# Kernel optimization log

Measured on AMD Instinct MI355X. Metric: run time of the kernel, lower is better.

## Reference

```python
import jax, jax.numpy as jnp
import numpy as np

B, T, C, H = 2, 2048, 1024, 16
HD = C // H  # head dim = 64


def setup_inputs() -> dict:
    key = jax.random.key(0)
    ks = jax.random.split(key, 5)
    s = 0.02  # GPT-style init scale for weights
    return {
        "x": jax.random.normal(ks[0], (B, T, C), dtype=jnp.float32),
        "Wq": jax.random.normal(ks[1], (C, C), dtype=jnp.float32) * s,
        "bq": jnp.zeros((C,), dtype=jnp.float32),
        "Wk": jax.random.normal(ks[2], (C, C), dtype=jnp.float32) * s,
        "bk": jnp.zeros((C,), dtype=jnp.float32),
        "Wv": jax.random.normal(ks[3], (C, C), dtype=jnp.float32) * s,
        "bv": jnp.zeros((C,), dtype=jnp.float32),
        "Wp": jax.random.normal(ks[4], (C, C), dtype=jnp.float32) * s,
        "bp": jnp.zeros((C,), dtype=jnp.float32),
    }


def reference(x, Wq, bq, Wk, bk, Wv, bv, Wp, bp):
    b, t, c = x.shape
    # torch nn.Linear: y = x @ W.T + b  (W is [out, in])
    def heads(W, bias):
        y = jnp.einsum("btc,oc->bto", x, W) + bias
        return y.reshape(b, t, H, HD).transpose(0, 2, 1, 3)  # [B,H,T,hd]

    q = heads(Wq, bq)
    k = heads(Wk, bk)
    v = heads(Wv, bv)

    scale = 1.0 / np.sqrt(HD).astype(np.float32)
    att = jnp.einsum("bhqd,bhkd->bhqk", q, k) * scale  # [B,H,T,T]
    causal = jnp.tril(jnp.ones((t, t), dtype=bool))
    att = jnp.where(causal[None, None], att, -jnp.inf)
    att = jax.nn.softmax(att, axis=-1)
    # attn_pdrop = 0.0 -> dropout is identity
    y = jnp.einsum("bhqk,bhkd->bhqd", att, v)  # [B,H,T,hd]
    y = y.transpose(0, 2, 1, 3).reshape(b, t, c)
    y = jnp.einsum("btc,oc->bto", y, Wp) + bp  # resid_pdrop = 0.0
    return y
```

## Files before the change

### kernel.cpp

```cpp
#include <hip/hip_runtime.h>
#include <hip/hip_bf16.h>

using bf16 = __hip_bfloat16;
typedef __attribute__((ext_vector_type(8))) short short8;
typedef __attribute__((ext_vector_type(4))) float floatx4;

#define B_  2
#define T_  2048
#define C_  1024
#define H_  16
#define HD_ 64
#define BT_ (B_*T_)
#define NX_ ((size_t)BT_*C_)
#define NW_ ((size_t)C_*C_)
#define PSTR2 40
#define KSCQ 0.1803368801f

__device__ __forceinline__ void gl2lds16(const bf16* g, bf16* l) {
    __builtin_amdgcn_global_load_lds((const __attribute__((address_space(1))) unsigned int*)g,
                                     (__attribute__((address_space(3))) unsigned int*)l,
                                     16, 0, 0);
}

__global__ __launch_bounds__(256) void cvt_f32_bf16(
    const float* __restrict__ x,
    const float* __restrict__ Wq, const float* __restrict__ Wk,
    const float* __restrict__ Wv, const float* __restrict__ Wp,
    bf16* __restrict__ xb, bf16* __restrict__ wqb, bf16* __restrict__ wkb,
    bf16* __restrict__ wvb, bf16* __restrict__ wpb)
{
    size_t i4 = ((size_t)blockIdx.x * 256 + threadIdx.x) * 4;
    const float* src; bf16* dst; size_t off;
    if (i4 < NX_) { src = x; dst = xb; off = i4; }
    else {
        size_t j = i4 - NX_;
        int r = (int)(j >> 20);
        off = j & (NW_ - 1);
        src = (r==0) ? Wq : (r==1) ? Wk : (r==2) ? Wv : Wp;
        dst = (r==0) ? wqb : (r==1) ? wkb : (r==2) ? wvb : wpb;
    }
    float4 v = *(const float4*)(src + off);
    union { bf16 h[4]; uint2 u; } o;
    o.h[0] = __float2bfloat16(v.x); o.h[1] = __float2bfloat16(v.y);
    o.h[2] = __float2bfloat16(v.z); o.h[3] = __float2bfloat16(v.w);
    *(uint2*)(dst + off) = o.u;
}

__global__ __launch_bounds__(256) void qkv_gemm(
    const bf16* __restrict__ x,
    const bf16* __restrict__ Wq, const float* __restrict__ bq,
    const bf16* __restrict__ Wk, const float* __restrict__ bk,
    const bf16* __restrict__ Wv, const float* __restrict__ bv,
    bf16* __restrict__ qo, bf16* __restrict__ ko, bf16* __restrict__ vt)
{
    __shared__ __align__(16) bf16 As[128*32];
    __shared__ __align__(16) bf16 Bs[128*32];

    const int tid  = threadIdx.x;
    const int w    = tid >> 6, lane = tid & 63;
    const int g    = lane >> 4, c16 = lane & 15;
    const int wr   = w >> 1,    wc  = w & 1;
    const int mtile = blockIdx.x, ntile = blockIdx.y;
    const int wsel  = ntile >> 3;
    const bf16*  W    = (wsel==0) ? Wq : (wsel==1 ? Wk : Wv);
    const float* bias = (wsel==0) ? bq : (wsel==1 ? bk : bv);
    const float oscale = (wsel==0) ? KSCQ : 1.0f;
    const int nbase  = (ntile & 7) * 128;

    const bf16* ag = x + (size_t)(mtile*128)*C_;
    const bf16* bg = W + (size_t)nbase*C_;

    floatx4 acc[4][4] = {};

    for (int k0 = 0; k0 < C_; k0 += 32) {
        #pragma unroll
        for (int p = 0; p < 2; ++p) {
            int cb = p*256 + w*64;
            int c  = cb + lane;
            gl2lds16(ag + (size_t)(c>>2)*C_ + k0 + (c&3)*8, As + cb*8);
            gl2lds16(bg + (size_t)(c>>2)*C_ + k0 + (c&3)*8, Bs + cb*8);
        }
        __syncthreads();

        short8 af[4], bfr[4];
        #pragma unroll
        for (int i = 0; i < 4; ++i)
            af[i] = *(const short8*)(As + (wr*64 + i*16 + c16)*32 + g*8);
        #pragma unroll
        for (int j = 0; j < 4; ++j)
            bfr[j] = *(const short8*)(Bs + (wc*64 + j*16 + c16)*32 + g*8);
        #pragma unroll
        for (int i = 0; i < 4; ++i)
            #pragma unroll
            for (int j = 0; j < 4; ++j)
                acc[i][j] = __builtin_amdgcn_mfma_f32_16x16x32_bf16(af[i], bfr[j], acc[i][j], 0, 0, 0);
        __syncthreads();
    }

    #pragma unroll
    for (int i = 0; i < 4; ++i) {
        int m0 = mtile*128 + wr*64 + i*16 + g*4;
        #pragma unroll
        for (int j = 0; j < 4; ++j) {
            int n = nbase + wc*64 + j*16 + c16;
            float bvf = bias[n];
            if (wsel == 2) {
                int bb = m0 >> 11, t0 = m0 & (T_-1);
                int hh = n >> 6,  hd = n & 63;
                union { bf16 hv[4]; uint2 u; } tmp;
                #pragma unroll
                for (int r = 0; r < 4; ++r) tmp.hv[r] = __float2bfloat16(acc[i][j][r] + bvf);
                *(uint2*)(vt + ((size_t)((bb*H_ + hh)*64 + hd))*T_ + t0) = tmp.u;
            } else {
                bf16* dst = (wsel==0) ? qo : ko;
                #pragma unroll
                for (int r = 0; r < 4; ++r)
                    dst[(size_t)(m0+r)*C_ + n] = __float2bfloat16((acc[i][j][r] + bvf) * oscale);
            }
        }
    }
}

__global__ __launch_bounds__(256, 4) void attn(
    const bf16* __restrict__ q, const bf16* __restrict__ k,
    const bf16* __restrict__ vt, bf16* __restrict__ y)
{
    __shared__ __align__(16) bf16 Ks[16*512];
    __shared__ __align__(16) bf16 Vs[16*512];
    __shared__ __align__(16) bf16 Ps[4][16*PSTR2];

    const int tid = threadIdx.x, w = tid >> 6, lane = tid & 63;
    const int g = lane >> 4, c16 = lane & 15;
    const int beta = blockIdx.x;
    const int p = beta & 15;
    const int h = (beta >> 4) & 15;
    const int b = beta >> 8;

    const bf16* kbase = k  + ((size_t)(b*T_))*C_ + h*64;
    const bf16* vbase = vt + ((size_t)(b*H_ + h))*64*T_;

    const short ONEB = 0x3F80;
    const short8 ones = {ONEB,ONEB,ONEB,ONEB,ONEB,ONEB,ONEB,ONEB};

    for (int ph = 0; ph < 2; ++ph) {
        const int qt = ph ? 31 - p : p;
        const int qbase = qt*64 + w*16;
        const int nit = (qt + 2) >> 1;
        const int qglob = qbase + c16;

        short8 aq[2];
        #pragma unroll
        for (int kg = 0; kg < 2; ++kg)
            aq[kg] = *(const short8*)(q + ((size_t)(b*T_ + qglob))*C_ + h*64 + kg*32 + g*8);

        floatx4 accO[4] = {};
        floatx4 lacc = {};

        for (int kt = 0; kt < nit; ++kt) {
            #pragma unroll
            for (int p2 = 0; p2 < 4; ++p2) {
                int f = w*4 + p2;
                int ctk = f >> 1, kg = f & 1;
                gl2lds16(kbase + (size_t)(kt*128 + ctk*16 + c16)*C_ + kg*32 + g*8, Ks + f*512);
                gl2lds16(vbase + (size_t)(p2*16 + c16)*T_ + kt*128 + w*32 + g*8,   Vs + f*512);
            }
            __syncthreads();

            floatx4 s[8];
            #pragma unroll
            for (int ct = 0; ct < 8; ++ct) {
                floatx4 a = {0.f, 0.f, 0.f, 0.f};
                #pragma unroll
                for (int kg = 0; kg < 2; ++kg) {
                    short8 kb = *(const short8*)(Ks + (ct*2 + kg)*512 + lane*8);
                    a = __builtin_amdgcn_mfma_f32_16x16x32_bf16(kb, aq[kg], a, 0, 0, 0);
                }
                s[ct] = a;
            }

            if (kt == nit-1) {
                #pragma unroll
                for (int ct = 0; ct < 8; ++ct)
                    #pragma unroll
                    for (int r = 0; r < 4; ++r) {
                        int key = kt*128 + ct*16 + g*4 + r;
                        if (key > qglob) s[ct][r] = -1e30f;
                    }
            }

            #pragma unroll
            for (int ks = 0; ks < 4; ++ks) {
                #pragma unroll
                for (int half = 0; half < 2; ++half) {
                    int ct = ks*2 + half;
                    float p0 = exp2f(s[ct][0]);
                    float p1 = exp2f(s[ct][1]);
                    float p2 = exp2f(s[ct][2]);
                    float p3 = exp2f(s[ct][3]);
                    union { __hip_bfloat162 h2[2]; uint2 u; } pk;
                    pk.h2[0] = __float22bfloat162_rn(float2{p0, p1});
                    pk.h2[1] = __float22bfloat162_rn(float2{p2, p3});
                    *(uint2*)(Ps[w] + c16*PSTR2 + half*16 + g*4) = pk.u;
                }
                short8 pa = *(const short8*)(Ps[w] + c16*PSTR2 + g*8);
                lacc = __builtin_amdgcn_mfma_f32_16x16x32_bf16(pa, ones, lacc, 0, 0, 0);
                #pragma unroll
                for (int nt = 0; nt < 4; ++nt) {
                    short8 vb = *(const short8*)(Vs + (ks*4 + nt)*512 + lane*8);
                    accO[nt] = __builtin_amdgcn_mfma_f32_16x16x32_bf16(pa, vb, accO[nt], 0, 0, 0);
                }
            }
            __syncthreads();
        }

        float ir[4];
        #pragma unroll
        for (int r = 0; r < 4; ++r) ir[r] = __builtin_amdgcn_rcpf(lacc[r]);
        #pragma unroll
        for (int nt = 0; nt < 4; ++nt)
            #pragma unroll
            for (int r = 0; r < 4; ++r) {
                int row = qbase + g*4 + r;
                float o = accO[nt][r] * ir[r];
                y[((size_t)(b*T_ + row))*C_ + h*64 + nt*16 + c16] = __float2bfloat16(o);
            }
    }
}

__global__ __launch_bounds__(256) void proj_gemm(
    const bf16* __restrict__ yin, const bf16* __restrict__ Wp, const float* __restrict__ bp,
    float* __restrict__ out)
{
    __shared__ __align__(16) bf16 As[64*32];
    __shared__ __align__(16) bf16 Bs[128*32];

    const int tid = threadIdx.x;
    const int w = tid >> 6, lane = tid & 63;
    const int g = lane >> 4, c16 = lane & 15;
    const int mtile = blockIdx.x, ntile = blockIdx.y;
    const int nbase = ntile * 128;

    const bf16* ag = yin + (size_t)(mtile*64)*C_;
    const bf16* bg = Wp  + (size_t)nbase*C_;

    floatx4 acc[4][2] = {};

    for (int k0 = 0; k0 < C_; k0 += 32) {
        gl2lds16(ag + (size_t)(w*16 + (lane>>2))*C_ + k0 + (lane&3)*8, As + w*512);
        #pragma unroll
        for (int p = 0; p < 2; ++p) {
            int cb = p*256 + w*64;
            int c  = cb + lane;
            gl2lds16(bg + (size_t)(c>>2)*C_ + k0 + (c&3)*8, Bs + cb*8);
        }
        __syncthreads();

        short8 af[4], bfr[2];
        #pragma unroll
        for (int i = 0; i < 4; ++i)
            af[i] = *(const short8*)(As + (i*16 + c16)*32 + g*8);
        #pragma unroll
        for (int j = 0; j < 2; ++j)
            bfr[j] = *(const short8*)(Bs + (w*32 + j*16 + c16)*32 + g*8);
        #pragma unroll
        for (int i = 0; i < 4; ++i)
            #pragma unroll
            for (int j = 0; j < 2; ++j)
                acc[i][j] = __builtin_amdgcn_mfma_f32_16x16x32_bf16(af[i], bfr[j], acc[i][j], 0, 0, 0);
        __syncthreads();
    }

    #pragma unroll
    for (int i = 0; i < 4; ++i) {
        int m0 = mtile*64 + i*16 + g*4;
        #pragma unroll
        for (int j = 0; j < 2; ++j) {
            int n = nbase + w*32 + j*16 + c16;
            float bvf = bp[n];
            #pragma unroll
            for (int r = 0; r < 4; ++r)
                out[(size_t)(m0+r)*C_ + n] = acc[i][j][r] + bvf;
        }
    }
}

extern "C" void kernel_launch(void* const* d_in, const int* in_sizes, int n_in,
                              void* d_out, int out_size, void* d_ws, size_t ws_size,
                              hipStream_t stream) {
    const float* x  = (const float*)d_in[0];
    const float* Wq = (const float*)d_in[1];
    const float* bq = (const float*)d_in[2];
    const float* Wk = (const float*)d_in[3];
    const float* bk = (const float*)d_in[4];
    const float* Wv = (const float*)d_in[5];
    const float* bv = (const float*)d_in[6];
    const float* Wp = (const float*)d_in[7];
    const float* bp = (const float*)d_in[8];

    bf16* xb  = (bf16*)d_ws;
    bf16* wqb = xb  + NX_;
    bf16* wkb = wqb + NW_;
    bf16* wvb = wkb + NW_;
    bf16* wpb = wvb + NW_;
    bf16* qw  = wpb + NW_;
    bf16* kw  = qw  + NX_;
    bf16* vt  = kw  + NX_;
    bf16* yw  = vt  + NX_;

    const int cvt_blocks = (int)((NX_ + 4*NW_) / (4*256));
    cvt_f32_bf16<<<cvt_blocks, 256, 0, stream>>>(x, Wq, Wk, Wv, Wp, xb, wqb, wkb, wvb, wpb);
    qkv_gemm<<<dim3(32, 24), 256, 0, stream>>>(xb, wqb, bq, wkb, bk, wvb, bv, qw, kw, vt);
    attn    <<<512, 256, 0, stream>>>(qw, kw, vt, yw);
    proj_gemm<<<dim3(64, 8), 256, 0, stream>>>(yw, wpb, bp, (float*)d_out);
}
```

Baseline: 197.8 us.

## Split attention key tiles across two wave groups and remap blocks per XCD

The attention kernel moves from 256 to 512 threads per block. Each group of four waves now handles half of every 128-key tile, and the two groups' partial output and row-sum accumulators are combined through LDS before the store. Block indices are remapped so the blocks for a given batch-head land on the same XCD, which should improve L2 reuse of K/V. This doubles waves per block to hide latency, at the cost of an extra reduction with two more barriers per phase and reuse of the K/V LDS buffers as scratch space.

```diff
diff --git a/kernel.cpp b/kernel.cpp
--- a/kernel.cpp
+++ b/kernel.cpp
@@ -121,20 +121,24 @@
     }
 }
 
-__global__ __launch_bounds__(256, 4) void attn(
+__global__ __launch_bounds__(512, 4) void attn(
     const bf16* __restrict__ q, const bf16* __restrict__ k,
     const bf16* __restrict__ vt, bf16* __restrict__ y)
 {
     __shared__ __align__(16) bf16 Ks[16*512];
     __shared__ __align__(16) bf16 Vs[16*512];
-    __shared__ __align__(16) bf16 Ps[4][16*PSTR2];
+    __shared__ __align__(16) bf16 Ps[8][16*PSTR2];
 
     const int tid = threadIdx.x, w = tid >> 6, lane = tid & 63;
     const int g = lane >> 4, c16 = lane & 15;
-    const int beta = blockIdx.x;
-    const int p = beta & 15;
-    const int h = (beta >> 4) & 15;
-    const int b = beta >> 8;
+    const int wq = w & 3;
+    const int kh = w >> 2;
+
+    const int xcd = blockIdx.x & 7;
+    const int j   = blockIdx.x >> 3;
+    const int p   = j & 15;
+    const int bh  = (j >> 4) * 8 + xcd;
+    const int b = bh >> 4, h = bh & 15;
 
     const bf16* kbase = k  + ((size_t)(b*T_))*C_ + h*64;
     const bf16* vbase = vt + ((size_t)(b*H_ + h))*64*T_;
@@ -144,7 +148,7 @@
 
     for (int ph = 0; ph < 2; ++ph) {
         const int qt = ph ? 31 - p : p;
-        const int qbase = qt*64 + w*16;
+        const int qbase = qt*64 + wq*16;
         const int nit = (qt + 2) >> 1;
         const int qglob = qbase + c16;
 
@@ -158,38 +162,37 @@
 
         for (int kt = 0; kt < nit; ++kt) {
             #pragma unroll
-            for (int p2 = 0; p2 < 4; ++p2) {
-                int f = w*4 + p2;
-                int ctk = f >> 1, kg = f & 1;
-                gl2lds16(kbase + (size_t)(kt*128 + ctk*16 + c16)*C_ + kg*32 + g*8, Ks + f*512);
-                gl2lds16(vbase + (size_t)(p2*16 + c16)*T_ + kt*128 + w*32 + g*8,   Vs + f*512);
+            for (int e = 0; e < 2; ++e) {
+                int f = w*2 + e;
+                gl2lds16(kbase + (size_t)(kt*128 + (f>>1)*16 + c16)*C_ + (f&1)*32 + g*8, Ks + f*512);
+                gl2lds16(vbase + (size_t)((f&3)*16 + c16)*T_ + kt*128 + (f>>2)*32 + g*8, Vs + f*512);
             }
             __syncthreads();
 
-            floatx4 s[8];
-            #pragma unroll
-            for (int ct = 0; ct < 8; ++ct) {
+            floatx4 s[4];
+            #pragma unroll
+            for (int ct = 0; ct < 4; ++ct) {
+                int ce = kh*4 + ct;
+                short8 kb0 = *(const short8*)(Ks + (ce*2+0)*512 + lane*8);
+                short8 kb1 = *(const short8*)(Ks + (ce*2+1)*512 + lane*8);
                 floatx4 a = {0.f, 0.f, 0.f, 0.f};
-                #pragma unroll
-                for (int kg = 0; kg < 2; ++kg) {
-                    short8 kb = *(const short8*)(Ks + (ct*2 + kg)*512 + lane*8);
-                    a = __builtin_amdgcn_mfma_f32_16x16x32_bf16(kb, aq[kg], a, 0, 0, 0);
-                }
+                a = __builtin_amdgcn_mfma_f32_16x16x32_bf16(kb0, aq[0], a, 0, 0, 0);
+                a = __builtin_amdgcn_mfma_f32_16x16x32_bf16(kb1, aq[1], a, 0, 0, 0);
                 s[ct] = a;
             }
 
             if (kt == nit-1) {
                 #pragma unroll
-                for (int ct = 0; ct < 8; ++ct)
+                for (int ct = 0; ct < 4; ++ct)
                     #pragma unroll
                     for (int r = 0; r < 4; ++r) {
-                        int key = kt*128 + ct*16 + g*4 + r;
+                        int key = kt*128 + kh*64 + ct*16 + g*4 + r;
                         if (key > qglob) s[ct][r] = -1e30f;
                     }
             }
 
             #pragma unroll
-            for (int ks = 0; ks < 4; ++ks) {
+            for (int ks = 0; ks < 2; ++ks) {
                 #pragma unroll
                 for (int half = 0; half < 2; ++half) {
                     int ct = ks*2 + half;
@@ -206,24 +209,46 @@
                 lacc = __builtin_amdgcn_mfma_f32_16x16x32_bf16(pa, ones, lacc, 0, 0, 0);
                 #pragma unroll
                 for (int nt = 0; nt < 4; ++nt) {
-                    short8 vb = *(const short8*)(Vs + (ks*4 + nt)*512 + lane*8);
+                    short8 vb = *(const short8*)(Vs + ((kh*2 + ks)*4 + nt)*512 + lane*8);
                     accO[nt] = __builtin_amdgcn_mfma_f32_16x16x32_bf16(pa, vb, accO[nt], 0, 0, 0);
                 }
             }
             __syncthreads();
         }
 
-        float ir[4];
-        #pragma unroll
-        for (int r = 0; r < 4; ++r) ir[r] = __builtin_amdgcn_rcpf(lacc[r]);
-        #pragma unroll
-        for (int nt = 0; nt < 4; ++nt)
-            #pragma unroll
-            for (int r = 0; r < 4; ++r) {
-                int row = qbase + g*4 + r;
-                float o = accO[nt][r] * ir[r];
-                y[((size_t)(b*T_ + row))*C_ + h*64 + nt*16 + c16] = __float2bfloat16(o);
-            }
+        if (w >= 4) {
+            float* dstf = ((w < 6) ? (float*)Ks : (float*)Vs) + (w & 1)*1280 + lane*20;
+            #pragma unroll
+            for (int nt = 0; nt < 4; ++nt) *(floatx4*)(dstf + nt*4) = accO[nt];
+            *(floatx4*)(dstf + 16) = lacc;
+        }
+        __syncthreads();
+        if (w < 4) {
+            int pw = w + 4;
+            const float* srcf = ((pw < 6) ? (const float*)Ks : (const float*)Vs) + (pw & 1)*1280 + lane*20;
+            #pragma unroll
+            for (int nt = 0; nt < 4; ++nt) {
+                floatx4 o = *(const floatx4*)(srcf + nt*4);
+                #pragma unroll
+                for (int r = 0; r < 4; ++r) accO[nt][r] += o[r];
+            }
+            floatx4 lo = *(const floatx4*)(srcf + 16);
+            #pragma unroll
+            for (int r = 0; r < 4; ++r) lacc[r] += lo[r];
+
+            float ir[4];
+            #pragma unroll
+            for (int r = 0; r < 4; ++r) ir[r] = __builtin_amdgcn_rcpf(lacc[r]);
+            #pragma unroll
+            for (int nt = 0; nt < 4; ++nt)
+                #pragma unroll
+                for (int r = 0; r < 4; ++r) {
+                    int row = qbase + g*4 + r;
+                    float o = accO[nt][r] * ir[r];
+                    y[((size_t)(b*T_ + row))*C_ + h*64 + nt*16 + c16] = __float2bfloat16(o);
+                }
+        }
+        __syncthreads();
     }
 }
 
@@ -310,6 +335,6 @@
     const int cvt_blocks = (int)((NX_ + 4*NW_) / (4*256));
     cvt_f32_bf16<<<cvt_blocks, 256, 0, stream>>>(x, Wq, Wk, Wv, Wp, xb, wqb, wkb, wvb, wpb);
     qkv_gemm<<<dim3(32, 24), 256, 0, stream>>>(xb, wqb, bq, wkb, bk, wvb, bv, qw, kw, vt);
-    attn    <<<512, 256, 0, stream>>>(qw, kw, vt, yw);
+    attn    <<<512, 512, 0, stream>>>(qw, kw, vt, yw);
     proj_gemm<<<dim3(64, 8), 256, 0, stream>>>(yw, wpb, bp, (float*)d_out);
 }
```

Result: faster. 184.2 us (-6.9%).
